# Optimization experiments

Hardware: AMD Instinct MI355X
Metric: run time of the kernel (lower is better)

## Reference

```python
import jax, jax.numpy as jnp
import numpy as np
import math

B, S, E, NH = 1024, 16, 32, 4  # batch, seq, attn embed dim, heads
H = 64                          # lstm1 hidden; lstm2 hidden = H//2 = E


def _pos_encoding(s, d):
    pos = jnp.arange(s, dtype=jnp.float32)[:, None]
    div = jnp.exp(jnp.arange(0, d, 2, dtype=jnp.float32) * (-math.log(10000.0) / d))
    pe = jnp.zeros((s, d), jnp.float32)
    pe = pe.at[:, 0::2].set(jnp.sin(pos * div))
    pe = pe.at[:, 1::2].set(jnp.cos(pos * div))
    return pe


def _lstm(x, wih, whh, bih, bhh):
    # x: [B,S,in]; PyTorch gate order i,f,g,o; h0=c0=0
    b = x.shape[0]
    h_dim = whh.shape[1]
    xg = jnp.einsum('bsi,gi->bsg', x, wih) + bih + bhh  # precompute input contribution

    def step(carry, xt):
        h, c = carry
        g = xt + h @ whh.T
        i, f, gg, o = jnp.split(g, 4, axis=-1)
        c = jax.nn.sigmoid(f) * c + jax.nn.sigmoid(i) * jnp.tanh(gg)
        h = jax.nn.sigmoid(o) * jnp.tanh(c)
        return (h, c), h

    h0 = jnp.zeros((b, h_dim), x.dtype)
    _, hs = jax.lax.scan(step, (h0, h0), jnp.swapaxes(xg, 0, 1))
    return jnp.swapaxes(hs, 0, 1)  # [B,S,H]


def setup_inputs() -> dict:
    key = jax.random.key(0)
    ks = jax.random.split(key, 24)

    def rn(k, shape, s=0.15):
        return jax.random.normal(k, shape, jnp.float32) * s

    return {
        'x': jax.random.normal(ks[0], (B, S, 1), jnp.float32),
        'emb_w': rn(ks[1], (32, 1)), 'emb_b': rn(ks[2], (32,), 0.05),
        'l1_wih': rn(ks[3], (4 * H, 32)), 'l1_whh': rn(ks[4], (4 * H, H)),
        'l1_bih': rn(ks[5], (4 * H,), 0.05), 'l1_bhh': rn(ks[6], (4 * H,), 0.05),
        'l2_wih': rn(ks[7], (4 * (H // 2), H)), 'l2_whh': rn(ks[8], (4 * (H // 2), H // 2)),
        'l2_bih': rn(ks[9], (4 * (H // 2),), 0.05), 'l2_bhh': rn(ks[10], (4 * (H // 2),), 0.05),
        'attn_w': rn(ks[11], (3 * E, E)), 'attn_b': rn(ks[12], (3 * E,), 0.05),
        'attn_ow': rn(ks[13], (E, E)), 'attn_ob': rn(ks[14], (E,), 0.05),
        'd1_w': rn(ks[15], (64, E)), 'd1_b': rn(ks[16], (64,), 0.05),
        'bn1_g': jnp.ones((64,), jnp.float32), 'bn1_b': jnp.zeros((64,), jnp.float32),
        'd2_w': rn(ks[17], (32, 64)), 'd2_b': rn(ks[18], (32,), 0.05),
        'bn2_g': jnp.ones((32,), jnp.float32), 'bn2_b': jnp.zeros((32,), jnp.float32),
        'd3_w': rn(ks[19], (1, 32)), 'd3_b': rn(ks[20], (1,), 0.05),
    }


def reference(x, emb_w, emb_b, l1_wih, l1_whh, l1_bih, l1_bhh,
              l2_wih, l2_whh, l2_bih, l2_bhh,
              attn_w, attn_b, attn_ow, attn_ob,
              d1_w, d1_b, bn1_g, bn1_b, d2_w, d2_b, bn2_g, bn2_b, d3_w, d3_b):
    eps = 1e-5
    h = x @ emb_w.T + emb_b                      # [B,S,32]
    h = h + _pos_encoding(h.shape[1], h.shape[2])
    l1 = _lstm(h, l1_wih, l1_whh, l1_bih, l1_bhh)          # [B,S,64]  (dropout: eval -> id)
    l2 = _lstm(l1, l2_wih, l2_whh, l2_bih, l2_bhh)         # [B,S,32]
    l2 = l2 + l1[:, :, :l2.shape[2]]                        # residual

    # nn.MultiheadAttention with default batch_first=False: attends over axis 0 (=B here),
    # faithful to the original module's behavior.
    L, N, _ = l2.shape
    hd = E // NH
    qkv = l2 @ attn_w.T + attn_b
    q, k, v = jnp.split(qkv, 3, axis=-1)
    q = q.reshape(L, N, NH, hd) * (1.0 / math.sqrt(hd))
    k = k.reshape(L, N, NH, hd)
    v = v.reshape(L, N, NH, hd)
    scores = jnp.einsum('lnhd,mnhd->nhlm', q, k)           # [S,4,B,B]
    a = jax.nn.softmax(scores, axis=-1)
    att = jnp.einsum('nhlm,mnhd->lnhd', a, v).reshape(L, N, E)
    att = att @ attn_ow.T + attn_ob

    z = att[:, -1, :]                                       # [B,32]

    def bn(t, g, b):  # eval-mode BatchNorm1d with fresh running stats (mean=0, var=1)
        return t * (g / jnp.sqrt(1.0 + eps)) + b

    z = jax.nn.relu(bn(z @ d1_w.T + d1_b, bn1_g, bn1_b))
    z = jax.nn.relu(bn(z @ d2_w.T + d2_b, bn2_g, bn2_b))
    return jax.nn.sigmoid(z @ d3_w.T + d3_b)                # [B,1]
```

## Files before the change

kernel.cpp:

```cpp
#include <hip/hip_runtime.h>
#include <math.h>


typedef __attribute__((ext_vector_type(8))) short short8v;
typedef __attribute__((ext_vector_type(4))) float f32x4;

__device__ __forceinline__ float sigf(float x) {
    float e = __expf(-x);
    return __builtin_amdgcn_rcpf(1.0f + e);
}
__device__ __forceinline__ float tanh_f(float x) {
    float a = fabsf(x);
    float e = __expf(2.0f * a);
    float t = 1.0f - 2.0f * __builtin_amdgcn_rcpf(e + 1.0f);
    return copysignf(t, x);
}
__device__ __forceinline__ unsigned short f2bf(float f) {
    unsigned int u = __float_as_uint(f);
    unsigned int r = (u + 0x7FFFu + ((u >> 16) & 1u)) >> 16;
    return (unsigned short)r;
}
__device__ __forceinline__ unsigned cvtpk_bf16(float lo, float hi) {
    unsigned r;
    asm("v_cvt_pk_bf16_f32 %0, %1, %2" : "=v"(r) : "v"(lo), "v"(hi));
    return r;
}

__global__ __launch_bounds__(256, 1) void lstm_kernel(
    const float* __restrict__ x,
    const float* __restrict__ emb_w, const float* __restrict__ emb_b,
    const float* __restrict__ wih1, const float* __restrict__ whh1,
    const float* __restrict__ bih1, const float* __restrict__ bhh1,
    const float* __restrict__ wih2, const float* __restrict__ whh2,
    const float* __restrict__ bih2, const float* __restrict__ bhh2,
    const float* __restrict__ attn_w, const float* __restrict__ attn_b,
    float* __restrict__ Q, float* __restrict__ K, float* __restrict__ V) {
    const int tid = threadIdx.x;
    const int w = tid >> 6, lane = tid & 63;
    const int l15 = lane & 15, q4 = lane >> 4;
    const int base = blockIdx.x * 16;

    __shared__ __align__(16) unsigned char E_raw[16 * 1024];
    __shared__ __align__(16) unsigned char H1_raw[2][2048];
    __shared__ __align__(16) unsigned char H2_raw[2][1024];
    __shared__ __align__(16) unsigned char WF2[24 * 1024];
    __shared__ __align__(16) float L1F[16][64];
    __shared__ __align__(16) float L2F[16][32];

    const unsigned jx7 = (unsigned)(l15 & 7) << 4;
    const unsigned jx4 = (unsigned)(l15 & 3) << 4;

    short8v w1f[4][3];
#pragma unroll
    for (int t = 0; t < 4; t++) {
        const int row = (w + 4 * t) * 16 + l15;
#pragma unroll
        for (int sl = 0; sl < 3; sl++) {
            short8v f;
#pragma unroll
            for (int e = 0; e < 8; e++) {
                int k = sl * 32 + q4 * 8 + e;
                float v = (k < 64) ? whh1[row * 64 + k] : wih1[row * 32 + (k - 64)];
                f[e] = (short)f2bf(v);
            }
            w1f[t][sl] = f;
        }
    }

    for (int f = w; f < 24; f += 4) {
        int t2 = f / 3, sl = f - t2 * 3;
        int row = t2 * 16 + l15;
        int koff = sl * 32 + q4 * 8;
        const float* src = (sl < 2) ? (wih2 + row * 64 + koff) : (whh2 + row * 32 + (koff - 64));
        float4 va = *(const float4*)(src);
        float4 vb = *(const float4*)(src + 4);
        short8v pk;
        pk[0] = (short)f2bf(va.x); pk[1] = (short)f2bf(va.y);
        pk[2] = (short)f2bf(va.z); pk[3] = (short)f2bf(va.w);
        pk[4] = (short)f2bf(vb.x); pk[5] = (short)f2bf(vb.y);
        pk[6] = (short)f2bf(vb.z); pk[7] = (short)f2bf(vb.w);
        *(short8v*)(&WF2[f * 1024 + lane * 16]) = pk;
    }

    float b1r[4][4];
#pragma unroll
    for (int t = 0; t < 4; t++)
#pragma unroll
        for (int e = 0; e < 4; e++) {
            int r = (w + 4 * t) * 16 + q4 * 4 + e;
            b1r[t][e] = bih1[r] + bhh1[r];
        }
    float b2r[4][4];
#pragma unroll
    for (int t = 0; t < 4; t++)
#pragma unroll
        for (int e = 0; e < 4; e++) {
            int r = ((w & 1) + 2 * t) * 16 + q4 * 4 + e;
            b2r[t][e] = bih2[r] + bhh2[r];
        }

    *(unsigned long long*)(H1_raw[1] + tid * 8) = 0ULL;
    if (tid < 128) *(unsigned long long*)(H2_raw[1] + tid * 8) = 0ULL;
    {
        const int je = tid >> 4, se = tid & 15;
        float xv = x[(base + je) * 16 + se];
        float ev[32];
#pragma unroll
        for (int ii = 0; ii < 16; ii++) {
            float d = __expf(-0.28782313662425574f * (float)(2 * ii));
            float ang = (float)se * d;
            ev[2 * ii] = xv * emb_w[2 * ii] + emb_b[2 * ii] + __sinf(ang);
            ev[2 * ii + 1] = xv * emb_w[2 * ii + 1] + emb_b[2 * ii + 1] + __cosf(ang);
        }
        unsigned jm = (unsigned)(je & 3) << 4;
#pragma unroll
        for (int b = 0; b < 4; b++) {
            short8v pk;
#pragma unroll
            for (int e = 0; e < 8; e++) pk[e] = (short)f2bf(ev[b * 8 + e]);
            *(short8v*)(&E_raw[se * 1024 + je * 64 + (((unsigned)(b * 16)) ^ jm)]) = pk;
        }
    }
    float c1[4] = {0.f, 0.f, 0.f, 0.f};
    float c2[4] = {0.f, 0.f, 0.f, 0.f};

    const int u0 = w * 16 + q4 * 4;

#define LDBE(S)  (*(const short8v*)(&E_raw[(S) * 1024] + (((unsigned)(l15 * 64 + q4 * 16)) ^ jx4)))
#define LDB0(HP) (*(const short8v*)((HP) + (((unsigned)(l15 * 128 + q4 * 16)) ^ jx7)))
#define LDB1(HP) (*(const short8v*)((HP) + (((unsigned)(l15 * 128 + 64 + q4 * 16)) ^ jx7)))
#define LDC2(HP) (*(const short8v*)((HP) + (((unsigned)(l15 * 64 + q4 * 16)) ^ jx4)))

    __syncthreads();

    short8v w2r[12];
#pragma unroll
    for (int t = 0; t < 4; t++)
#pragma unroll
        for (int sl = 0; sl < 3; sl++)
            w2r[t * 3 + sl] =
                *(const short8v*)(&WF2[((((w & 1) + 2 * t) * 3 + sl) << 10) + lane * 16]);

    auto phase1 = [&](unsigned char* H1n, short8v BE, short8v B0, short8v B1, bool last) {
        f32x4 a0 = {b1r[0][0], b1r[0][1], b1r[0][2], b1r[0][3]};
        f32x4 a1 = {b1r[1][0], b1r[1][1], b1r[1][2], b1r[1][3]};
        f32x4 a2 = {b1r[2][0], b1r[2][1], b1r[2][2], b1r[2][3]};
        f32x4 a3 = {b1r[3][0], b1r[3][1], b1r[3][2], b1r[3][3]};
        a0 = __builtin_amdgcn_mfma_f32_16x16x32_bf16(w1f[0][2], BE, a0, 0, 0, 0);
        a1 = __builtin_amdgcn_mfma_f32_16x16x32_bf16(w1f[1][2], BE, a1, 0, 0, 0);
        a2 = __builtin_amdgcn_mfma_f32_16x16x32_bf16(w1f[2][2], BE, a2, 0, 0, 0);
        a3 = __builtin_amdgcn_mfma_f32_16x16x32_bf16(w1f[3][2], BE, a3, 0, 0, 0);
        a0 = __builtin_amdgcn_mfma_f32_16x16x32_bf16(w1f[0][0], B0, a0, 0, 0, 0);
        a1 = __builtin_amdgcn_mfma_f32_16x16x32_bf16(w1f[1][0], B0, a1, 0, 0, 0);
        a2 = __builtin_amdgcn_mfma_f32_16x16x32_bf16(w1f[2][0], B0, a2, 0, 0, 0);
        a3 = __builtin_amdgcn_mfma_f32_16x16x32_bf16(w1f[3][0], B0, a3, 0, 0, 0);
        a0 = __builtin_amdgcn_mfma_f32_16x16x32_bf16(w1f[0][1], B1, a0, 0, 0, 0);
        a1 = __builtin_amdgcn_mfma_f32_16x16x32_bf16(w1f[1][1], B1, a1, 0, 0, 0);
        a2 = __builtin_amdgcn_mfma_f32_16x16x32_bf16(w1f[2][1], B1, a2, 0, 0, 0);
        a3 = __builtin_amdgcn_mfma_f32_16x16x32_bf16(w1f[3][1], B1, a3, 0, 0, 0);
        float h1v[4];
#pragma unroll
        for (int e = 0; e < 4; e++) {
            c1[e] = sigf(a1[e]) * c1[e] + sigf(a0[e]) * tanh_f(a2[e]);
            h1v[e] = sigf(a3[e]) * tanh_f(c1[e]);
        }
        uint2 pk = make_uint2(cvtpk_bf16(h1v[0], h1v[1]), cvtpk_bf16(h1v[2], h1v[3]));
        *(uint2*)(H1n + (((unsigned)(l15 * 128 + u0 * 2)) ^ jx7)) = pk;
        if (last) *(float4*)(&L1F[l15][u0]) = make_float4(h1v[0], h1v[1], h1v[2], h1v[3]);
    };

    phase1(H1_raw[0], LDBE(0), LDB0(H1_raw[1]), LDB1(H1_raw[1]), false);

#pragma unroll 2
    for (int s = 0; s < 16; s++) {
        const int p = s & 1;
        __syncthreads();
        short8v B0 = LDB0(H1_raw[p]);
        short8v B1 = LDB1(H1_raw[p]);
        short8v BEn = LDBE((s < 15) ? (s + 1) : 15);
        short8v C2 = LDC2(H2_raw[p ^ 1]);
        if (w < 2) {
            f32x4 d0 = {b2r[0][0], b2r[0][1], b2r[0][2], b2r[0][3]};
            f32x4 d1 = {b2r[1][0], b2r[1][1], b2r[1][2], b2r[1][3]};
            f32x4 d2 = {b2r[2][0], b2r[2][1], b2r[2][2], b2r[2][3]};
            f32x4 d3 = {b2r[3][0], b2r[3][1], b2r[3][2], b2r[3][3]};
            d0 = __builtin_amdgcn_mfma_f32_16x16x32_bf16(w2r[0], B0, d0, 0, 0, 0);
            d1 = __builtin_amdgcn_mfma_f32_16x16x32_bf16(w2r[3], B0, d1, 0, 0, 0);
            d2 = __builtin_amdgcn_mfma_f32_16x16x32_bf16(w2r[6], B0, d2, 0, 0, 0);
            d3 = __builtin_amdgcn_mfma_f32_16x16x32_bf16(w2r[9], B0, d3, 0, 0, 0);
            d0 = __builtin_amdgcn_mfma_f32_16x16x32_bf16(w2r[1], B1, d0, 0, 0, 0);
            d1 = __builtin_amdgcn_mfma_f32_16x16x32_bf16(w2r[4], B1, d1, 0, 0, 0);
            d2 = __builtin_amdgcn_mfma_f32_16x16x32_bf16(w2r[7], B1, d2, 0, 0, 0);
            d3 = __builtin_amdgcn_mfma_f32_16x16x32_bf16(w2r[10], B1, d3, 0, 0, 0);
            d0 = __builtin_amdgcn_mfma_f32_16x16x32_bf16(w2r[2], C2, d0, 0, 0, 0);
            d1 = __builtin_amdgcn_mfma_f32_16x16x32_bf16(w2r[5], C2, d1, 0, 0, 0);
            d2 = __builtin_amdgcn_mfma_f32_16x16x32_bf16(w2r[8], C2, d2, 0, 0, 0);
            d3 = __builtin_amdgcn_mfma_f32_16x16x32_bf16(w2r[11], C2, d3, 0, 0, 0);
            float h2v[4];
#pragma unroll
            for (int e = 0; e < 4; e++) {
                c2[e] = sigf(d1[e]) * c2[e] + sigf(d0[e]) * tanh_f(d2[e]);
                h2v[e] = sigf(d3[e]) * tanh_f(c2[e]);
            }
            uint2 pk = make_uint2(cvtpk_bf16(h2v[0], h2v[1]), cvtpk_bf16(h2v[2], h2v[3]));
            *(uint2*)(H2_raw[p] + (((unsigned)(l15 * 64 + u0 * 2)) ^ jx4)) = pk;
            if (s == 15) *(float4*)(&L2F[l15][u0]) = make_float4(h2v[0], h2v[1], h2v[2], h2v[3]);
        }
        if (s < 15) phase1(H1_raw[p ^ 1], BEn, B0, B1, (s + 1) == 15);
    }

    __syncthreads();
    {
        const int j = tid >> 4, rb = tid & 15;
        const int gb = base + j;
        const float4* l1p = (const float4*)(&L1F[j][0]);
        const float4* l2p = (const float4*)(&L2F[j][0]);
#pragma unroll
        for (int rep = 0; rep < 6; rep++) {
            int row = rb + 16 * rep;
            float acc = attn_b[row];
            const float4* wrow = (const float4*)(attn_w + row * 32);
#pragma unroll
            for (int k4 = 0; k4 < 8; k4++) {
                float4 lv1 = l1p[k4];
                float4 lv2 = l2p[k4];
                float4 ww = wrow[k4];
                float lx = lv2.x + lv1.x, ly = lv2.y + lv1.y, lz = lv2.z + lv1.z, lw = lv2.w + lv1.w;
                acc += lx * ww.x + ly * ww.y + lz * ww.z + lw * ww.w;
            }
            if (row < 32) Q[gb * 32 + row] = acc * 0.35355339059327373f;
            else if (row < 64) K[gb * 32 + (row - 32)] = acc;
            else V[gb * 32 + (row - 64)] = acc;
        }
    }
#undef LDBE
#undef LDB0
#undef LDB1
#undef LDC2
}

__global__ __launch_bounds__(256, 2) void attn_kernel(
    const float* __restrict__ Q, const float* __restrict__ K, const float* __restrict__ V,
    float* __restrict__ pm, float* __restrict__ ps, float* __restrict__ pacc) {
    int c = blockIdx.x & 15, lt = blockIdx.x >> 4;
    int t = threadIdx.x;
    int h = t >> 6, l = lt * 64 + (t & 63);
    __shared__ __align__(16) float Ks[64 * 32];
    __shared__ __align__(16) float Vs[64 * 32];
    {
        const float4* Kg = (const float4*)(K + c * 2048);
        const float4* Vg = (const float4*)(V + c * 2048);
        float4* K4 = (float4*)Ks;
        float4* V4 = (float4*)Vs;
        K4[t] = Kg[t];
        K4[t + 256] = Kg[t + 256];
        V4[t] = Vg[t];
        V4[t + 256] = Vg[t + 256];
    }
    const float4* qg = (const float4*)(Q + l * 32 + h * 8);
    float4 q0 = qg[0], q1 = qg[1];
    __syncthreads();
    float m_r = -1e30f, l_r = 0.f;
    float4 acc0 = {0, 0, 0, 0}, acc1 = {0, 0, 0, 0};
#pragma unroll 4
    for (int m = 0; m < 64; m++) {
        const float4* k4 = (const float4*)(Ks + m * 32 + h * 8);
        float4 ka = k4[0], kb = k4[1];
        float s = q0.x * ka.x + q0.y * ka.y + q0.z * ka.z + q0.w * ka.w +
                  q1.x * kb.x + q1.y * kb.y + q1.z * kb.z + q1.w * kb.w;
        const float4* v4 = (const float4*)(Vs + m * 32 + h * 8);
        float4 va = v4[0], vb = v4[1];
        float nm = fmaxf(m_r, s);
        float f = __expf(m_r - nm);
        float pp = __expf(s - nm);
        l_r = l_r * f + pp;
        acc0.x = acc0.x * f + pp * va.x;
        acc0.y = acc0.y * f + pp * va.y;
        acc0.z = acc0.z * f + pp * va.z;
        acc0.w = acc0.w * f + pp * va.w;
        acc1.x = acc1.x * f + pp * vb.x;
        acc1.y = acc1.y * f + pp * vb.y;
        acc1.z = acc1.z * f + pp * vb.z;
        acc1.w = acc1.w * f + pp * vb.w;
        m_r = nm;
    }
    int idx = (c * 4 + h) * 1024 + l;
    pm[idx] = m_r;
    ps[idx] = l_r;
    float4* po = (float4*)(pacc + idx * 8);
    po[0] = acc0;
    po[1] = acc1;
}

__global__ __launch_bounds__(256) void head_kernel(
    const float* __restrict__ pm, const float* __restrict__ ps, const float* __restrict__ pacc,
    const float* __restrict__ ow, const float* __restrict__ ob,
    const float* __restrict__ d1w, const float* __restrict__ d1b,
    const float* __restrict__ g1, const float* __restrict__ b1,
    const float* __restrict__ d2w, const float* __restrict__ d2b,
    const float* __restrict__ g2, const float* __restrict__ b2,
    const float* __restrict__ d3w, const float* __restrict__ d3b,
    float* __restrict__ out) {
    int wid = threadIdx.x >> 6, j = threadIdx.x & 63;
    int l = blockIdx.x * 4 + wid;
    __shared__ float att_s[4][32], z_s[4][32], r1s[4][64];
    if (j < 32) {
        int h = j >> 3, d = j & 7;
        float M = -1e30f;
#pragma unroll
        for (int c = 0; c < 16; c++) M = fmaxf(M, pm[(c * 4 + h) * 1024 + l]);
        float den = 0.f, num = 0.f;
#pragma unroll
        for (int c = 0; c < 16; c++) {
            int idx = (c * 4 + h) * 1024 + l;
            float e = __expf(pm[idx] - M);
            den += e * ps[idx];
            num += e * pacc[idx * 8 + d];
        }
        att_s[wid][j] = num / den;
    }
    __syncthreads();
    if (j < 32) {
        float a = ob[j];
        const float4* aw = (const float4*)(&att_s[wid][0]);
        const float4* wr = (const float4*)(ow + j * 32);
#pragma unroll
        for (int k4 = 0; k4 < 8; k4++) {
            float4 u = aw[k4], wv = wr[k4];
            a += u.x * wv.x + u.y * wv.y + u.z * wv.z + u.w * wv.w;
        }
        z_s[wid][j] = a;
    }
    __syncthreads();
    const float inv = rsqrtf(1.0f + 1e-5f);
    {
        float a = d1b[j];
        const float4* zw = (const float4*)(&z_s[wid][0]);
        const float4* wr = (const float4*)(d1w + j * 32);
#pragma unroll
        for (int k4 = 0; k4 < 8; k4++) {
            float4 u = zw[k4], wv = wr[k4];
            a += u.x * wv.x + u.y * wv.y + u.z * wv.z + u.w * wv.w;
        }
        a = a * (g1[j] * inv) + b1[j];
        r1s[wid][j] = fmaxf(a, 0.f);
    }
    __syncthreads();
    if (j < 32) {
        float a = d2b[j];
        const float4* rw = (const float4*)(&r1s[wid][0]);
        const float4* wr = (const float4*)(d2w + j * 64);
#pragma unroll
        for (int k4 = 0; k4 < 16; k4++) {
            float4 u = rw[k4], wv = wr[k4];
            a += u.x * wv.x + u.y * wv.y + u.z * wv.z + u.w * wv.w;
        }
        a = a * (g2[j] * inv) + b2[j];
        float r2 = fmaxf(a, 0.f);
        float p = r2 * d3w[j];
        p += __shfl_down(p, 16);
        p += __shfl_down(p, 8);
        p += __shfl_down(p, 4);
        p += __shfl_down(p, 2);
        p += __shfl_down(p, 1);
        if (j == 0) out[l] = __builtin_amdgcn_rcpf(1.0f + __expf(-(p + d3b[0])));
    }
}

extern "C" void kernel_launch(void* const* d_in, const int* in_sizes, int n_in,
                              void* d_out, int out_size, void* d_ws, size_t ws_size,
                              hipStream_t stream) {
    const float* x      = (const float*)d_in[0];
    const float* emb_w  = (const float*)d_in[1];
    const float* emb_b  = (const float*)d_in[2];
    const float* l1_wih = (const float*)d_in[3];
    const float* l1_whh = (const float*)d_in[4];
    const float* l1_bih = (const float*)d_in[5];
    const float* l1_bhh = (const float*)d_in[6];
    const float* l2_wih = (const float*)d_in[7];
    const float* l2_whh = (const float*)d_in[8];
    const float* l2_bih = (const float*)d_in[9];
    const float* l2_bhh = (const float*)d_in[10];
    const float* attn_w = (const float*)d_in[11];
    const float* attn_b = (const float*)d_in[12];
    const float* attn_ow = (const float*)d_in[13];
    const float* attn_ob = (const float*)d_in[14];
    const float* d1_w  = (const float*)d_in[15];
    const float* d1_b  = (const float*)d_in[16];
    const float* bn1_g = (const float*)d_in[17];
    const float* bn1_b = (const float*)d_in[18];
    const float* d2_w  = (const float*)d_in[19];
    const float* d2_b  = (const float*)d_in[20];
    const float* bn2_g = (const float*)d_in[21];
    const float* bn2_b = (const float*)d_in[22];
    const float* d3_w  = (const float*)d_in[23];
    const float* d3_b  = (const float*)d_in[24];
    float* out = (float*)d_out;

    float* ws   = (float*)d_ws;
    float* Q    = ws;
    float* K    = ws + 32768;
    float* V    = ws + 65536;
    float* pm   = ws + 98304;
    float* ps   = ws + 163840;
    float* pacc = ws + 229376;

    lstm_kernel<<<64, 256, 0, stream>>>(x, emb_w, emb_b, l1_wih, l1_whh, l1_bih, l1_bhh,
                                        l2_wih, l2_whh, l2_bih, l2_bhh,
                                        attn_w, attn_b, Q, K, V);
    attn_kernel<<<256, 256, 0, stream>>>(Q, K, V, pm, ps, pacc);
    head_kernel<<<256, 256, 0, stream>>>(pm, ps, pacc, attn_ow, attn_ob, d1_w, d1_b,
                                         bn1_g, bn1_b, d2_w, d2_b, bn2_g, bn2_b,
                                         d3_w, d3_b, out);
}
```

Baseline: 142.4 us.

## Split LSTM1 step into MFMA and activation parts, interleave with uniform LSTM2 work

The layer-1 LSTM step is split into separate MFMA and activation lambdas. The loop now issues layer-2 MFMAs, then layer-1 MFMAs, then both activation blocks, so matrix work overlaps transcendental math. The w<2 branch is removed: all waves compute layer-2 gates and only the store stays predicated. This avoids wave divergence and lets the scheduler interleave the two layers. The cost is redundant layer-2 MFMA and activation work on waves 2-3, plus an unconditional layer-1 step at s=15 whose H1 output is written but never used. Weights are held as f32x4 behind an asm barrier so they stay pinned in VGPRs.

Result: no change. 141.0 us (-1.0%).

```diff
diff --git a/kernel.cpp b/kernel.cpp
--- a/kernel.cpp
+++ b/kernel.cpp
@@ -133,19 +133,23 @@
 
     __syncthreads();
 
-    short8v w2r[12];
+    f32x4 w2rf[12];
 #pragma unroll
     for (int t = 0; t < 4; t++)
 #pragma unroll
         for (int sl = 0; sl < 3; sl++)
-            w2r[t * 3 + sl] =
-                *(const short8v*)(&WF2[((((w & 1) + 2 * t) * 3 + sl) << 10) + lane * 16]);
-
-    auto phase1 = [&](unsigned char* H1n, short8v BE, short8v B0, short8v B1, bool last) {
-        f32x4 a0 = {b1r[0][0], b1r[0][1], b1r[0][2], b1r[0][3]};
-        f32x4 a1 = {b1r[1][0], b1r[1][1], b1r[1][2], b1r[1][3]};
-        f32x4 a2 = {b1r[2][0], b1r[2][1], b1r[2][2], b1r[2][3]};
-        f32x4 a3 = {b1r[3][0], b1r[3][1], b1r[3][2], b1r[3][3]};
+            w2rf[t * 3 + sl] =
+                *(const f32x4*)(&WF2[((((w & 1) + 2 * t) * 3 + sl) << 10) + lane * 16]);
+#pragma unroll
+    for (int i = 0; i < 12; i++) asm volatile("" : "+v"(w2rf[i]));
+#define W2R(I) (__builtin_bit_cast(short8v, w2rf[I]))
+
+    auto p1_mfma = [&](short8v BE, short8v B0, short8v B1,
+                       f32x4& a0, f32x4& a1, f32x4& a2, f32x4& a3) {
+        a0 = {b1r[0][0], b1r[0][1], b1r[0][2], b1r[0][3]};
+        a1 = {b1r[1][0], b1r[1][1], b1r[1][2], b1r[1][3]};
+        a2 = {b1r[2][0], b1r[2][1], b1r[2][2], b1r[2][3]};
+        a3 = {b1r[3][0], b1r[3][1], b1r[3][2], b1r[3][3]};
         a0 = __builtin_amdgcn_mfma_f32_16x16x32_bf16(w1f[0][2], BE, a0, 0, 0, 0);
         a1 = __builtin_amdgcn_mfma_f32_16x16x32_bf16(w1f[1][2], BE, a1, 0, 0, 0);
         a2 = __builtin_amdgcn_mfma_f32_16x16x32_bf16(w1f[2][2], BE, a2, 0, 0, 0);
@@ -158,6 +162,9 @@
         a1 = __builtin_amdgcn_mfma_f32_16x16x32_bf16(w1f[1][1], B1, a1, 0, 0, 0);
         a2 = __builtin_amdgcn_mfma_f32_16x16x32_bf16(w1f[2][1], B1, a2, 0, 0, 0);
         a3 = __builtin_amdgcn_mfma_f32_16x16x32_bf16(w1f[3][1], B1, a3, 0, 0, 0);
+    };
+    auto p1_act = [&](f32x4 a0, f32x4 a1, f32x4 a2, f32x4 a3,
+                      unsigned char* H1n, bool wrL1F) {
         float h1v[4];
 #pragma unroll
         for (int e = 0; e < 4; e++) {
@@ -166,10 +173,14 @@
         }
         uint2 pk = make_uint2(cvtpk_bf16(h1v[0], h1v[1]), cvtpk_bf16(h1v[2], h1v[3]));
         *(uint2*)(H1n + (((unsigned)(l15 * 128 + u0 * 2)) ^ jx7)) = pk;
-        if (last) *(float4*)(&L1F[l15][u0]) = make_float4(h1v[0], h1v[1], h1v[2], h1v[3]);
+        if (wrL1F) *(float4*)(&L1F[l15][u0]) = make_float4(h1v[0], h1v[1], h1v[2], h1v[3]);
     };
 
-    phase1(H1_raw[0], LDBE(0), LDB0(H1_raw[1]), LDB1(H1_raw[1]), false);
+    {
+        f32x4 a0, a1, a2, a3;
+        p1_mfma(LDBE(0), LDB0(H1_raw[1]), LDB1(H1_raw[1]), a0, a1, a2, a3);
+        p1_act(a0, a1, a2, a3, H1_raw[0], false);
+    }
 
 #pragma unroll 2
     for (int s = 0; s < 16; s++) {
@@ -179,23 +190,25 @@
         short8v B1 = LDB1(H1_raw[p]);
         short8v BEn = LDBE((s < 15) ? (s + 1) : 15);
         short8v C2 = LDC2(H2_raw[p ^ 1]);
-        if (w < 2) {
-            f32x4 d0 = {b2r[0][0], b2r[0][1], b2r[0][2], b2r[0][3]};
-            f32x4 d1 = {b2r[1][0], b2r[1][1], b2r[1][2], b2r[1][3]};
-            f32x4 d2 = {b2r[2][0], b2r[2][1], b2r[2][2], b2r[2][3]};
-            f32x4 d3 = {b2r[3][0], b2r[3][1], b2r[3][2], b2r[3][3]};
-            d0 = __builtin_amdgcn_mfma_f32_16x16x32_bf16(w2r[0], B0, d0, 0, 0, 0);
-            d1 = __builtin_amdgcn_mfma_f32_16x16x32_bf16(w2r[3], B0, d1, 0, 0, 0);
-            d2 = __builtin_amdgcn_mfma_f32_16x16x32_bf16(w2r[6], B0, d2, 0, 0, 0);
-            d3 = __builtin_amdgcn_mfma_f32_16x16x32_bf16(w2r[9], B0, d3, 0, 0, 0);
-            d0 = __builtin_amdgcn_mfma_f32_16x16x32_bf16(w2r[1], B1, d0, 0, 0, 0);
-            d1 = __builtin_amdgcn_mfma_f32_16x16x32_bf16(w2r[4], B1, d1, 0, 0, 0);
-            d2 = __builtin_amdgcn_mfma_f32_16x16x32_bf16(w2r[7], B1, d2, 0, 0, 0);
-            d3 = __builtin_amdgcn_mfma_f32_16x16x32_bf16(w2r[10], B1, d3, 0, 0, 0);
-            d0 = __builtin_amdgcn_mfma_f32_16x16x32_bf16(w2r[2], C2, d0, 0, 0, 0);
-            d1 = __builtin_amdgcn_mfma_f32_16x16x32_bf16(w2r[5], C2, d1, 0, 0, 0);
-            d2 = __builtin_amdgcn_mfma_f32_16x16x32_bf16(w2r[8], C2, d2, 0, 0, 0);
-            d3 = __builtin_amdgcn_mfma_f32_16x16x32_bf16(w2r[11], C2, d3, 0, 0, 0);
+        f32x4 d0 = {b2r[0][0], b2r[0][1], b2r[0][2], b2r[0][3]};
+        f32x4 d1 = {b2r[1][0], b2r[1][1], b2r[1][2], b2r[1][3]};
+        f32x4 d2 = {b2r[2][0], b2r[2][1], b2r[2][2], b2r[2][3]};
+        f32x4 d3 = {b2r[3][0], b2r[3][1], b2r[3][2], b2r[3][3]};
+        d0 = __builtin_amdgcn_mfma_f32_16x16x32_bf16(W2R(0), B0, d0, 0, 0, 0);
+        d1 = __builtin_amdgcn_mfma_f32_16x16x32_bf16(W2R(3), B0, d1, 0, 0, 0);
+        d2 = __builtin_amdgcn_mfma_f32_16x16x32_bf16(W2R(6), B0, d2, 0, 0, 0);
+        d3 = __builtin_amdgcn_mfma_f32_16x16x32_bf16(W2R(9), B0, d3, 0, 0, 0);
+        d0 = __builtin_amdgcn_mfma_f32_16x16x32_bf16(W2R(1), B1, d0, 0, 0, 0);
+        d1 = __builtin_amdgcn_mfma_f32_16x16x32_bf16(W2R(4), B1, d1, 0, 0, 0);
+        d2 = __builtin_amdgcn_mfma_f32_16x16x32_bf16(W2R(7), B1, d2, 0, 0, 0);
+        d3 = __builtin_amdgcn_mfma_f32_16x16x32_bf16(W2R(10), B1, d3, 0, 0, 0);
+        d0 = __builtin_amdgcn_mfma_f32_16x16x32_bf16(W2R(2), C2, d0, 0, 0, 0);
+        d1 = __builtin_amdgcn_mfma_f32_16x16x32_bf16(W2R(5), C2, d1, 0, 0, 0);
+        d2 = __builtin_amdgcn_mfma_f32_16x16x32_bf16(W2R(8), C2, d2, 0, 0, 0);
+        d3 = __builtin_amdgcn_mfma_f32_16x16x32_bf16(W2R(11), C2, d3, 0, 0, 0);
+        f32x4 a0, a1, a2, a3;
+        p1_mfma(BEn, B0, B1, a0, a1, a2, a3);
+        {
             float h2v[4];
 #pragma unroll
             for (int e = 0; e < 4; e++) {
@@ -203,10 +216,13 @@
                 h2v[e] = sigf(d3[e]) * tanh_f(c2[e]);
             }
             uint2 pk = make_uint2(cvtpk_bf16(h2v[0], h2v[1]), cvtpk_bf16(h2v[2], h2v[3]));
-            *(uint2*)(H2_raw[p] + (((unsigned)(l15 * 64 + u0 * 2)) ^ jx4)) = pk;
-            if (s == 15) *(float4*)(&L2F[l15][u0]) = make_float4(h2v[0], h2v[1], h2v[2], h2v[3]);
-        }
-        if (s < 15) phase1(H1_raw[p ^ 1], BEn, B0, B1, (s + 1) == 15);
+            if (w < 2) {
+                *(uint2*)(H2_raw[p] + (((unsigned)(l15 * 64 + u0 * 2)) ^ jx4)) = pk;
+                if (s == 15) *(float4*)(&L2F[l15][u0]) =
+                    make_float4(h2v[0], h2v[1], h2v[2], h2v[3]);
+            }
+        }
+        p1_act(a0, a1, a2, a3, H1_raw[p ^ 1], s == 14);
     }
 
     __syncthreads();
@@ -237,6 +253,7 @@
 #undef LDB0
 #undef LDB1
 #undef LDC2
+#undef W2R
 }
 
 __global__ __launch_bounds__(256, 2) void attn_kernel(
```
